# Kernel tuning notes

Hardware: AMD Instinct MI355X
Metric: run time of the kernel (lower is better)

The kernel has to match this reference:

```python
import jax, jax.numpy as jnp
import numpy as np

B, S = 64, 512
NQ, RAW, D, H, K = 10000, 256, 256, 64, 4  # vocab, raw emb, model emb, gru state, num_stages
LN_EPS = 1e-5


def setup_inputs() -> dict:
    key = jax.random.key(0)
    ks = jax.random.split(key, 30)
    def n(i, shape, s=0.02):
        return (jax.random.normal(ks[i], shape) * s).astype(jnp.float32)
    return {
        "q": jax.random.randint(ks[0], (B, S), 0, NQ, dtype=jnp.int32),
        "r": jax.random.randint(ks[1], (B, S), 0, 2, dtype=jnp.int32),
        # flattened 4-stage embedding table [NQ*4, RAW]
        "emb_table": n(2, (NQ * K, RAW)),
        # per-stage expert MLPs (weights stored as [in, out])
        "expert_w1": n(3, (K, RAW, RAW)), "expert_b1": n(4, (K, RAW)),
        "expert_w2": n(5, (K, RAW, D)),  "expert_b2": n(6, (K, D)),
        # router input adapter Linear(RAW*4 -> D)
        "adapter_w": n(7, (RAW * K, D)), "adapter_b": n(8, (D,)),
        # interaction reducer Linear(2D -> H)
        "reducer_w": n(9, (2 * D, H)), "reducer_b": n(10, (H,)),
        "start_token": jnp.zeros((1, 1, H), jnp.float32),
        # torch GRU params: [3H, in], gate order (r, z, n)
        "gru_w_ih": n(11, (3 * H, H)), "gru_w_hh": n(12, (3 * H, H)),
        "gru_b_ih": n(13, (3 * H,)),   "gru_b_hh": n(14, (3 * H,)),
        # gate Linear(D+H -> 4)
        "wgate_w": n(15, (D + H, K)), "wgate_b": n(16, (K,)),
        "ln_gamma": jnp.ones((D,), jnp.float32), "ln_beta": jnp.zeros((D,), jnp.float32),
        "resp_table": n(17, (2, D)),
        "proj_cor_w": n(18, (D, D)), "proj_cor_b": n(19, (D,)),
        "proj_inc_w": n(20, (D, D)), "proj_inc_b": n(21, (D,)),
    }


def _forward(q, r, emb_table, expert_w1, expert_b1, expert_w2, expert_b2,
             adapter_w, adapter_b, reducer_w, reducer_b, start_token,
             gru_w_ih, gru_w_hh, gru_b_ih, gru_b_hh, wgate_w, wgate_b,
             ln_gamma, ln_beta, resp_table, proj_cor_w, proj_cor_b,
             proj_inc_w, proj_inc_b):
    b, s = q.shape
    # 4-stage embedding lookup: indices q*4 + [0..3]
    stage_idx = q[..., None] * K + jnp.arange(K)          # [B,S,4]
    q_raw = emb_table[stage_idx]                          # [B,S,4,RAW]
    # smart summary (router input adapter), eval mode -> no dropout
    q_flat = q_raw.reshape(b, s, K * RAW)
    q_summary = jax.nn.relu(q_flat @ adapter_w + adapter_b)  # [B,S,D]
    r_emb = resp_table[r]                                    # [B,S,D]
    gru_in = jnp.concatenate([q_summary, r_emb], -1) @ reducer_w + reducer_b  # [B,S,H]
    start = jnp.broadcast_to(start_token, (b, 1, H))
    x = jnp.concatenate([start, gru_in[:, :-1]], axis=1)     # shifted [B,S,H]
    # GRU over time (torch gate order r,z,n)
    xg = x @ gru_w_ih.T + gru_b_ih                           # [B,S,3H]
    def step(h, xg_t):
        hg = h @ gru_w_hh.T + gru_b_hh
        xr, xz, xn = jnp.split(xg_t, 3, axis=-1)
        hr, hz, hn = jnp.split(hg, 3, axis=-1)
        rg = jax.nn.sigmoid(xr + hr)
        zg = jax.nn.sigmoid(xz + hz)
        ng = jnp.tanh(xn + rg * hn)
        h_new = (1.0 - zg) * ng + zg * h
        return h_new, h_new
    _, m = jax.lax.scan(step, jnp.zeros((b, H), x.dtype), xg.transpose(1, 0, 2))
    m_seq = m.transpose(1, 0, 2)                             # [B,S,H]
    # parallel experts (vectorized over the 4 stages)
    h1 = jax.nn.relu(jnp.einsum('bske,keh->bskh', q_raw, expert_w1) + expert_b1)
    experts = jnp.einsum('bskh,khd->bskd', h1, expert_w2) + expert_b2  # [B,S,4,D]
    # noisy routing (eval: no noise), top-1 mask, softmax gating
    logits = jnp.concatenate([q_summary, m_seq], -1) @ wgate_w + wgate_b  # [B,S,4]
    gate_probs = jax.nn.softmax(logits, axis=-1)
    top1 = jnp.argmax(logits, axis=-1)
    onehot = jax.nn.one_hot(top1, K, dtype=logits.dtype)
    masked = jnp.where(onehot > 0, logits, -jnp.inf)
    gate_w = jax.nn.softmax(masked, axis=-1)                 # one-hot for top_k=1
    combined = jnp.einsum('bskd,bsk->bsd', experts, gate_w)  # [B,S,D]
    # layer norm
    mu = combined.mean(-1, keepdims=True)
    var = combined.var(-1, keepdims=True)
    q_fused = ln_gamma * (combined - mu) * jax.lax.rsqrt(var + LN_EPS) + ln_beta
    emb_cor = q_fused @ proj_cor_w + proj_cor_b
    emb_inc = q_fused @ proj_inc_w + proj_inc_b
    rm = r[..., None].astype(q_fused.dtype)
    qa_fused = emb_cor * rm + emb_inc * (1.0 - rm)
    return q_fused, qa_fused, gate_probs


def reference(q, r, emb_table, expert_w1, expert_b1, expert_w2, expert_b2,
              adapter_w, adapter_b, reducer_w, reducer_b, start_token,
              gru_w_ih, gru_w_hh, gru_b_ih, gru_b_hh, wgate_w, wgate_b,
              ln_gamma, ln_beta, resp_table, proj_cor_w, proj_cor_b,
              proj_inc_w, proj_inc_b):
    q_fused, qa_fused, _ = _forward(q, r, emb_table, expert_w1, expert_b1,
                                    expert_w2, expert_b2, adapter_w, adapter_b,
                                    reducer_w, reducer_b, start_token,
                                    gru_w_ih, gru_w_hh, gru_b_ih, gru_b_hh,
                                    wgate_w, wgate_b, ln_gamma, ln_beta,
                                    resp_table, proj_cor_w, proj_cor_b,
                                    proj_inc_w, proj_inc_b)
    return (q_fused, qa_fused)
```

## Files before the change

### kernel.cpp

```cpp
#include <hip/hip_runtime.h>
#include <cstddef>


#define NQ 10000
#define TT 32768

typedef __attribute__((ext_vector_type(8))) short bf16x8;
typedef __attribute__((ext_vector_type(4))) float f32x4;

__device__ double g_qs  [NQ * 256];
__device__ double g_xgr [2 * 192];
__device__ float  g_xg0f[192];
__device__ float  g_xq2 [NQ * 384];
__device__ double g_lq  [NQ * 4];
__device__ float  g_m   [TT * 64];
__device__ int    g_top1[TT];
__device__ unsigned short g_w1t  [4 * 256 * 256];
__device__ unsigned short g_w2t  [4 * 256 * 256];
__device__ unsigned short g_projt[512 * 256];
__device__ unsigned short g_qf   [NQ * 4 * 256];

__device__ __forceinline__ float bf2f(unsigned short x) {
  return __uint_as_float(((unsigned)x) << 16);
}
__device__ __forceinline__ unsigned short f2bf(float f) {
  unsigned u = __float_as_uint(f);
  u += 0x7FFFu + ((u >> 16) & 1u);
  return (unsigned short)(u >> 16);
}
__device__ __forceinline__ f32x4 mfma16(bf16x8 a, bf16x8 b, f32x4 c) {
  return __builtin_amdgcn_mfma_f32_16x16x32_bf16(a, b, c, 0, 0, 0);
}
__device__ __forceinline__ void pkfma(float2& c, float2 a, float2 b) {
  asm("v_pk_fma_f32 %0, %1, %2, %0" : "+v"(c) : "v"(a), "v"(b));
}

__device__ __forceinline__ double fexp(double x) {
  const double L2E  = 1.4426950408889634074;
  const double LN2H = 6.93147180369123816490e-01;
  const double LN2L = 1.90821492927058770002e-10;
  double n = rint(x * L2E);
  int ni = (int)n;
  double r = fma(-n, LN2H, x);
  r = fma(-n, LN2L, r);
  double p = 2.7557319223985888e-07;
  p = fma(p, r, 2.7557319223985893e-06);
  p = fma(p, r, 2.4801587301587302e-05);
  p = fma(p, r, 1.9841269841269841e-04);
  p = fma(p, r, 1.3888888888888889e-03);
  p = fma(p, r, 8.3333333333333332e-03);
  p = fma(p, r, 4.1666666666666664e-02);
  p = fma(p, r, 1.6666666666666666e-01);
  p = fma(p, r, 0.5);
  p = fma(p, r, 1.0);
  p = fma(p, r, 1.0);
  return ldexp(p, ni);
}

__device__ __forceinline__ double tpoly(double p) {
  const double p2 = p * p;
  double t = -1382.0 / 155925.0;
  t = fma(t, p2, 62.0 / 2835.0);
  t = fma(t, p2, -17.0 / 315.0);
  t = fma(t, p2, 2.0 / 15.0);
  t = fma(t, p2, -1.0 / 3.0);
  t = fma(t, p2, 1.0);
  return p * t;
}

__global__ void __launch_bounds__(256) prep_kernel(
    const float* __restrict__ expert_w1, const float* __restrict__ expert_w2,
    const float* __restrict__ proj_cor_w, const float* __restrict__ proj_inc_w,
    const float* __restrict__ resp_table, const float* __restrict__ reducer_w,
    const float* __restrict__ reducer_b,  const float* __restrict__ start_token,
    const float* __restrict__ gru_w_ih,   const float* __restrict__ gru_b_ih)
{
  __shared__ double red2f[128];
  const int tid = threadIdx.x;
  if (blockIdx.x == 0) {
    if (tid < 128) {
      const int rr = tid >> 6, j = tid & 63;
      double acc = (double)reducer_b[j];
      for (int k = 0; k < 256; ++k)
        acc += (double)resp_table[rr * 256 + k] *
               (double)reducer_w[(256 + k) * 64 + j];
      red2f[tid] = acc;
    }
    __syncthreads();
    if (tid < 192) {
      const double bih = (double)gru_b_ih[tid];
      double a0 = bih, a1 = bih, a2 = bih;
      for (int j = 0; j < 64; ++j) {
        const double w = (double)gru_w_ih[tid * 64 + j];
        a0 += red2f[j] * w;
        a1 += red2f[64 + j] * w;
        a2 += (double)start_token[j] * w;
      }
      g_xgr[tid] = a0; g_xgr[192 + tid] = a1; g_xg0f[tid] = (float)a2;
    }
  }
  const int idx0 = blockIdx.x * 256 + tid;
  const int stride = gridDim.x * 256;
  for (int i = idx0; i < 4 * 256 * 256; i += stride) {
    const int e = i >> 16, rem = i & 65535, n = rem >> 8, k = rem & 255;
    g_w1t[i] = f2bf(expert_w1[e * 65536 + k * 256 + n]);
    g_w2t[i] = f2bf(expert_w2[e * 65536 + k * 256 + n]);
  }
  for (int i = idx0; i < 512 * 256; i += stride) {
    const int n = i >> 8, k = i & 255;
    g_projt[i] = f2bf((n < 256) ? proj_cor_w[k * 256 + n]
                                : proj_inc_w[k * 256 + (n - 256)]);
  }
}

__global__ void __launch_bounds__(256) qsk_kernel(
    const float* __restrict__ emb, const float* __restrict__ adapter_w,
    const float* __restrict__ adapter_b)
{
  __shared__ __align__(16) float As[64][33];
  __shared__ __align__(16) float Bs[32][65];
  const int tid = threadIdx.x;
  const int q0 = blockIdx.x * 64;
  const int n0 = blockIdx.y * 64;
  const int ty = tid >> 4, tx = tid & 15;

  double acc[4][4];
#pragma unroll
  for (int i = 0; i < 4; ++i)
#pragma unroll
    for (int j = 0; j < 4; ++j) acc[i][j] = 0.0;

  const int arow = tid >> 2, aks = (tid & 3) * 8;
  const int qa = min(q0 + arow, NQ - 1);
  const int bkk = tid >> 3, bns = (tid & 7) * 8;

  for (int kc = 0; kc < 1024; kc += 32) {
    f32x4 av0 = *(const f32x4*)(emb + (size_t)qa * 1024 + kc + aks);
    f32x4 av1 = *(const f32x4*)(emb + (size_t)qa * 1024 + kc + aks + 4);
    f32x4 bv0 = *(const f32x4*)(adapter_w + (size_t)(kc + bkk) * 256 + n0 + bns);
    f32x4 bv1 = *(const f32x4*)(adapter_w + (size_t)(kc + bkk) * 256 + n0 + bns + 4);
    __syncthreads();
#pragma unroll
    for (int i = 0; i < 4; ++i) { As[arow][aks + i] = av0[i]; As[arow][aks + 4 + i] = av1[i]; }
#pragma unroll
    for (int i = 0; i < 4; ++i) { Bs[bkk][bns + i] = bv0[i]; Bs[bkk][bns + 4 + i] = bv1[i]; }
    __syncthreads();
#pragma unroll 4
    for (int kk = 0; kk < 32; ++kk) {
      double a[4], b[4];
#pragma unroll
      for (int i = 0; i < 4; ++i) a[i] = (double)As[ty * 4 + i][kk];
#pragma unroll
      for (int j = 0; j < 4; ++j) b[j] = (double)Bs[kk][tx * 4 + j];
#pragma unroll
      for (int i = 0; i < 4; ++i)
#pragma unroll
        for (int j = 0; j < 4; ++j) acc[i][j] = fma(a[i], b[j], acc[i][j]);
    }
  }
#pragma unroll
  for (int i = 0; i < 4; ++i) {
    const int qrow = q0 + ty * 4 + i;
    if (qrow < NQ) {
#pragma unroll
      for (int j = 0; j < 4; ++j) {
        const int n = n0 + tx * 4 + j;
        double v = acc[i][j] + (double)adapter_b[n];
        g_qs[(size_t)qrow * 256 + n] = v > 0.0 ? v : 0.0;
      }
    }
  }
}

__global__ void __launch_bounds__(256) smallk_kernel(
    const float* __restrict__ reducer_w, const float* __restrict__ gru_w_ih,
    const float* __restrict__ wgate_w)
{
  __shared__ double qsr[256];
  __shared__ double ps[4][64];
  __shared__ double gi[64];
  const int tid = threadIdx.x;
  const int qq = blockIdx.x;
  qsr[tid] = g_qs[(size_t)qq * 256 + tid];
  __syncthreads();
  {
    const int j = tid & 63, h = tid >> 6;
    const int k0 = h * 64;
    double a0 = 0.0, a1 = 0.0, a2 = 0.0, a3 = 0.0;
    for (int k = 0; k < 64; k += 4) {
      a0 = fma(qsr[k0 + k + 0], (double)reducer_w[(k0 + k + 0) * 64 + j], a0);
      a1 = fma(qsr[k0 + k + 1], (double)reducer_w[(k0 + k + 1) * 64 + j], a1);
      a2 = fma(qsr[k0 + k + 2], (double)reducer_w[(k0 + k + 2) * 64 + j], a2);
      a3 = fma(qsr[k0 + k + 3], (double)reducer_w[(k0 + k + 3) * 64 + j], a3);
    }
    ps[h][j] = (a0 + a1) + (a2 + a3);
  }
  __syncthreads();
  if (tid < 64) gi[tid] = (ps[0][tid] + ps[1][tid]) + (ps[2][tid] + ps[3][tid]);
  if (tid >= 64 && tid < 68) {
    const int e = tid - 64;
    double a0 = 0.0, a1 = 0.0, a2 = 0.0, a3 = 0.0;
    for (int k = 0; k < 256; k += 4) {
      a0 = fma(qsr[k + 0], (double)wgate_w[(k + 0) * 4 + e], a0);
      a1 = fma(qsr[k + 1], (double)wgate_w[(k + 1) * 4 + e], a1);
      a2 = fma(qsr[k + 2], (double)wgate_w[(k + 2) * 4 + e], a2);
      a3 = fma(qsr[k + 3], (double)wgate_w[(k + 3) * 4 + e], a3);
    }
    g_lq[(size_t)qq * 4 + e] = (a0 + a1) + (a2 + a3);
  }
  __syncthreads();
  if (tid < 192) {
    double a0 = 0.0, a1 = 0.0, a2 = 0.0, a3 = 0.0;
    for (int k = 0; k < 64; k += 4) {
      a0 = fma(gi[k + 0], (double)gru_w_ih[tid * 64 + k + 0], a0);
      a1 = fma(gi[k + 1], (double)gru_w_ih[tid * 64 + k + 1], a1);
      a2 = fma(gi[k + 2], (double)gru_w_ih[tid * 64 + k + 2], a2);
      a3 = fma(gi[k + 3], (double)gru_w_ih[tid * 64 + k + 3], a3);
    }
    const double s = (a0 + a1) + (a2 + a3);
    g_xq2[(size_t)qq * 384 + tid]       = (float)(s + g_xgr[tid]);
    g_xq2[(size_t)qq * 384 + 192 + tid] = (float)(s + g_xgr[192 + tid]);
  }
}

__global__ void __attribute__((amdgpu_waves_per_eu(1, 1)))
__launch_bounds__(128, 1) gru_kernel(
    const int* __restrict__ q, const int* __restrict__ r,
    const float* __restrict__ whh, const float* __restrict__ bhh)
{
  __shared__ __align__(16) float HF[2][68];
  const int tid = threadIdx.x;
  const int b = blockIdx.x;
  const int wv = tid >> 6;
  const int l = tid & 63;
  const int p = l >> 1;
  const int half = l & 1;
  const int j = wv * 32 + p;
  const int k0 = half * 32;

  float2 Wr[16], Wz[16], Wn[16];
#pragma unroll
  for (int i = 0; i < 16; ++i) {
    Wr[i] = *(const float2*)(whh + (size_t)(0 * 64 + j) * 64 + k0 + 2 * i);
    Wz[i] = *(const float2*)(whh + (size_t)(1 * 64 + j) * 64 + k0 + 2 * i);
    Wn[i] = *(const float2*)(whh + (size_t)(2 * 64 + j) * 64 + k0 + 2 * i);
  }
#pragma unroll
  for (int i = 0; i < 16; ++i) {
    asm volatile("" : "+v"(Wr[i]));
    asm volatile("" : "+v"(Wz[i]));
    asm volatile("" : "+v"(Wn[i]));
  }
  const double br = (double)bhh[j];
  const double bz = (double)bhh[64 + j];
  const double bn = (double)bhh[128 + j];

  float cx0 = g_xg0f[j], cx1 = g_xg0f[64 + j], cx2 = g_xg0f[128 + j];
  int qA = q[b * 512], rA = r[b * 512];

  const int jpad = j + ((j >> 5) << 2);
  if (tid < 64) {
    const int tp = tid + ((tid >> 5) << 2);
    HF[0][tp] = 0.f;
  }
  double hd = 0.0;
  asm volatile("s_waitcnt lgkmcnt(0)\n\ts_barrier" ::: "memory");

  for (int t = 0; t < 512; ++t) {
    float nx0 = 0.f, nx1 = 0.f, nx2 = 0.f;
    int qB = qA, rB = rA;
    if (t < 511) {
      const size_t base = (size_t)(qA * 2 + rA) * 192 + j;
      nx0 = g_xq2[base];
      nx1 = g_xq2[base + 64];
      nx2 = g_xq2[base + 128];
      const int tk = min(t + 1, 510);
      qB = q[b * 512 + tk];
      rB = r[b * 512 + tk];
    }

    float2 ar = {0.f, 0.f}, az = {0.f, 0.f}, an = {0.f, 0.f};
    {
      const float4* hp = (const float4*)&HF[t & 1][half * 36];
#pragma unroll
      for (int g = 0; g < 8; ++g) {
        const float4 t4 = hp[g];
        const float2 hA = make_float2(t4.x, t4.y);
        const float2 hB = make_float2(t4.z, t4.w);
        pkfma(ar, Wr[2 * g], hA); pkfma(ar, Wr[2 * g + 1], hB);
        pkfma(az, Wz[2 * g], hA); pkfma(az, Wz[2 * g + 1], hB);
        pkfma(an, Wn[2 * g], hA); pkfma(an, Wn[2 * g + 1], hB);
      }
    }
    const float srh = ar.x + ar.y;
    const float szh = az.x + az.y;
    const float snh = an.x + an.y;
    const float sro = __shfl_xor(srh, 1);
    const float szo = __shfl_xor(szh, 1);
    const float sno = __shfl_xor(snh, 1);
    const double hr = br + ((double)srh + (double)sro);
    const double hz = bz + ((double)szh + (double)szo);
    const double hn = bn + ((double)snh + (double)sno);
    const double pr = (double)cx0 + hr, pz = (double)cx1 + hz;
    const double xn = (double)cx2;
    double rg = fma(0.5, tpoly(0.5 * pr), 0.5);
    double zg = fma(0.5, tpoly(0.5 * pz), 0.5);
    double pre = fma(rg, hn, xn);
    double ng = tpoly(pre);
    const bool bad = (fabs(pr) > 0.5) | (fabs(pz) > 0.5) | (fabs(pre) > 0.25);
    if (bad) {
      rg = 1.0 / (1.0 + fexp(-pr));
      zg = 1.0 / (1.0 + fexp(-pz));
      pre = fma(rg, hn, xn);
      ng = 1.0 - 2.0 / (fexp(pre + pre) + 1.0);
    }
    const double hnew = fma(zg, hd - ng, ng);
    hd = hnew;
    const float hnf = (float)hnew;
    if (half == 0) {
      HF[(t & 1) ^ 1][jpad] = hnf;
      g_m[((size_t)b * 512 + t) * 64 + j] = hnf;
    }
    asm volatile("s_waitcnt lgkmcnt(0)\n\ts_barrier" ::: "memory");

    cx0 = nx0; cx1 = nx1; cx2 = nx2;
    qA = qB; rA = rB;
  }
}

__global__ void __launch_bounds__(256) top1_kernel(
    const int* __restrict__ q,
    const float* __restrict__ wgate_w, const float* __restrict__ wgate_b)
{
  __shared__ double w2[256];
  const int tid = threadIdx.x;
  w2[tid] = (double)wgate_w[1024 + tid];
  __syncthreads();
  const int t = blockIdx.x * 256 + tid;
  const int qv = q[t];
  double l0 = g_lq[(size_t)qv * 4 + 0] + (double)wgate_b[0];
  double l1 = g_lq[(size_t)qv * 4 + 1] + (double)wgate_b[1];
  double l2 = g_lq[(size_t)qv * 4 + 2] + (double)wgate_b[2];
  double l3 = g_lq[(size_t)qv * 4 + 3] + (double)wgate_b[3];
  const f32x4* mr4 = (const f32x4*)(g_m + (size_t)t * 64);
#pragma unroll 4
  for (int jj = 0; jj < 16; ++jj) {
    const f32x4 mv4 = mr4[jj];
#pragma unroll
    for (int c = 0; c < 4; ++c) {
      const double mv = (double)mv4[c];
      const int k = (jj * 4 + c) * 4;
      l0 = fma(mv, w2[k + 0], l0);
      l1 = fma(mv, w2[k + 1], l1);
      l2 = fma(mv, w2[k + 2], l2);
      l3 = fma(mv, w2[k + 3], l3);
    }
  }
  int bi = 0; double bvv = l0;
  if (l1 > bvv) { bvv = l1; bi = 1; }
  if (l2 > bvv) { bvv = l2; bi = 2; }
  if (l3 > bvv) { bvv = l3; bi = 3; }
  g_top1[t] = bi;
}

__global__ void __launch_bounds__(128) kernelE(
    const float* __restrict__ emb,
    const float* __restrict__ b1, const float* __restrict__ b2,
    const float* __restrict__ lng, const float* __restrict__ lnb)
{
  __shared__ __align__(16) unsigned short QR[32 * 264];
  __shared__ __align__(16) unsigned short H1[32 * 264];
  __shared__ __align__(16) unsigned short EO[32 * 264];
  const int tid = threadIdx.x;
  const int t0 = blockIdx.x * 32;
  const int e  = blockIdx.y;
  const int w = tid >> 6;
  const int lane = tid & 63;
  const int l15 = lane & 15;
  const int quad = lane >> 4;

  for (int c = 0; c < 16; ++c) {
    const int idx = c * 128 + tid;
    const int row = idx >> 6, col4 = idx & 63;
    const int qv = min(t0 + row, NQ - 1);
    f32x4 v = *(const f32x4*)(emb + (size_t)qv * 1024 + e * 256 + col4 * 4);
    unsigned a = ((unsigned)f2bf(v[1]) << 16) | f2bf(v[0]);
    unsigned bb = ((unsigned)f2bf(v[3]) << 16) | f2bf(v[2]);
    *(uint2*)&QR[row * 264 + col4 * 4] = make_uint2(a, bb);
  }
  __syncthreads();

  const f32x4 z4 = {0.f, 0.f, 0.f, 0.f};
  const int n0 = w * 128;

  f32x4 acc[2][8];
#pragma unroll
  for (int a = 0; a < 2; ++a)
#pragma unroll
    for (int bq = 0; bq < 8; ++bq) acc[a][bq] = z4;
#pragma unroll
  for (int ks = 0; ks < 8; ++ks) {
    const int koff = ks * 32 + quad * 8;
    bf16x8 a0 = *(const bf16x8*)&QR[l15 * 264 + koff];
    bf16x8 a1 = *(const bf16x8*)&QR[(16 + l15) * 264 + koff];
#pragma unroll
    for (int nt = 0; nt < 8; ++nt) {
      bf16x8 bbv = *(const bf16x8*)(g_w1t + (size_t)e * 65536 +
                                    (size_t)(n0 + nt * 16 + l15) * 256 + koff);
      acc[0][nt] = mfma16(a0, bbv, acc[0][nt]);
      acc[1][nt] = mfma16(a1, bbv, acc[1][nt]);
    }
  }
#pragma unroll
  for (int nt = 0; nt < 8; ++nt) {
    const int n = n0 + nt * 16 + l15;
    const float b1v = b1[e * 256 + n];
#pragma unroll
    for (int mt = 0; mt < 2; ++mt)
#pragma unroll
      for (int rg = 0; rg < 4; ++rg) {
        const int m = mt * 16 + quad * 4 + rg;
        H1[m * 264 + n] = f2bf(fmaxf(acc[mt][nt][rg] + b1v, 0.f));
      }
  }
  __syncthreads();

  f32x4 acc2[2][8];
#pragma unroll
  for (int a = 0; a < 2; ++a)
#pragma unroll
    for (int bq = 0; bq < 8; ++bq) acc2[a][bq] = z4;
#pragma unroll
  for (int ks = 0; ks < 8; ++ks) {
    const int koff = ks * 32 + quad * 8;
    bf16x8 a0 = *(const bf16x8*)&H1[l15 * 264 + koff];
    bf16x8 a1 = *(const bf16x8*)&H1[(16 + l15) * 264 + koff];
#pragma unroll
    for (int nt = 0; nt < 8; ++nt) {
      bf16x8 bbv = *(const bf16x8*)(g_w2t + (size_t)e * 65536 +
                                    (size_t)(n0 + nt * 16 + l15) * 256 + koff);
      acc2[0][nt] = mfma16(a0, bbv, acc2[0][nt]);
      acc2[1][nt] = mfma16(a1, bbv, acc2[1][nt]);
    }
  }
#pragma unroll
  for (int nt = 0; nt < 8; ++nt) {
    const int n = n0 + nt * 16 + l15;
    const float b2v = b2[e * 256 + n];
#pragma unroll
    for (int mt = 0; mt < 2; ++mt)
#pragma unroll
      for (int rg = 0; rg < 4; ++rg) {
        const int m = mt * 16 + quad * 4 + rg;
        EO[m * 264 + n] = f2bf(acc2[mt][nt][rg] + b2v);
      }
  }
  __syncthreads();

  {
    const int m = tid >> 2;
    const int sub = tid & 3;
    float sx = 0.f, sxx = 0.f;
#pragma unroll
    for (int i = 0; i < 8; ++i) {
      bf16x8 v = *(const bf16x8*)&EO[m * 264 + sub * 64 + i * 8];
#pragma unroll
      for (int c = 0; c < 8; ++c) {
        const float f = bf2f((unsigned short)v[c]);
        sx += f; sxx += f * f;
      }
    }
    sx += __shfl_xor(sx, 1); sxx += __shfl_xor(sxx, 1);
    sx += __shfl_xor(sx, 2); sxx += __shfl_xor(sxx, 2);
    const float mu = sx * (1.f / 256.f);
    const float var = sxx * (1.f / 256.f) - mu * mu;
    const float inv = 1.f / sqrtf(var + 1e-5f);
    if (t0 + m < NQ) {
      const size_t base = ((size_t)(t0 + m) * 4 + e) * 256;
#pragma unroll
      for (int i = 0; i < 8; ++i) {
        const int dbase = sub * 64 + i * 8;
        bf16x8 v = *(const bf16x8*)&EO[m * 264 + dbase];
        bf16x8 ov;
#pragma unroll
        for (int c = 0; c < 8; ++c) {
          const int d = dbase + c;
          const float f = bf2f((unsigned short)v[c]);
          ov[c] = (short)f2bf(lng[d] * (f - mu) * inv + lnb[d]);
        }
        *(bf16x8*)(g_qf + base + dbase) = ov;
      }
    }
  }
}

__global__ void __launch_bounds__(128) kernelF(
    const int* __restrict__ q, const int* __restrict__ r,
    const float* __restrict__ pcb, const float* __restrict__ pib,
    float* __restrict__ out)
{
  __shared__ __align__(16) unsigned short QF[32 * 264];
  __shared__ int rv_l[32];
  const int tid = threadIdx.x;
  const int t0 = blockIdx.x * 32;
  const int w = tid >> 6;
  const int lane = tid & 63;
  const int l15 = lane & 15;
  const int quad = lane >> 4;
  if (tid < 32) rv_l[tid] = r[t0 + tid];
  __syncthreads();

  {
    const int m = tid >> 2;
    const size_t row = ((size_t)q[t0 + m] * 4 + g_top1[t0 + m]) * 256;
#pragma unroll
    for (int i = 0; i < 8; ++i) {
      const int dbase = (tid & 3) * 64 + i * 8;
      bf16x8 v = *(const bf16x8*)(g_qf + row + dbase);
      *(bf16x8*)&QF[m * 264 + dbase] = v;
      f32x4 f0, f1;
#pragma unroll
      for (int c = 0; c < 4; ++c) f0[c] = bf2f((unsigned short)v[c]);
#pragma unroll
      for (int c = 0; c < 4; ++c) f1[c] = bf2f((unsigned short)v[4 + c]);
      *(f32x4*)(out + (size_t)(t0 + m) * 256 + dbase) = f0;
      *(f32x4*)(out + (size_t)(t0 + m) * 256 + dbase + 4) = f1;
    }
  }
  __syncthreads();

  const f32x4 z4 = {0.f, 0.f, 0.f, 0.f};
  const int n0 = w * 128;
  for (int ph = 0; ph < 2; ++ph) {
    f32x4 acc[2][8];
#pragma unroll
    for (int a = 0; a < 2; ++a)
#pragma unroll
      for (int bq = 0; bq < 8; ++bq) acc[a][bq] = z4;
#pragma unroll
    for (int ks = 0; ks < 8; ++ks) {
      const int koff = ks * 32 + quad * 8;
      bf16x8 a0 = *(const bf16x8*)&QF[l15 * 264 + koff];
      bf16x8 a1 = *(const bf16x8*)&QF[(16 + l15) * 264 + koff];
#pragma unroll
      for (int nt = 0; nt < 8; ++nt) {
        bf16x8 bbv = *(const bf16x8*)(g_projt +
            (size_t)(ph * 256 + n0 + nt * 16 + l15) * 256 + koff);
        acc[0][nt] = mfma16(a0, bbv, acc[0][nt]);
        acc[1][nt] = mfma16(a1, bbv, acc[1][nt]);
      }
    }
    const float* pbb = ph ? pib : pcb;
    const int want = ph ? 0 : 1;
#pragma unroll
    for (int nt = 0; nt < 8; ++nt) {
      const int n = n0 + nt * 16 + l15;
      const float pbv = pbb[n];
#pragma unroll
      for (int mt = 0; mt < 2; ++mt)
#pragma unroll
        for (int rg = 0; rg < 4; ++rg) {
          const int m = mt * 16 + quad * 4 + rg;
          if (rv_l[m] == want)
            out[(size_t)TT * 256 + (size_t)(t0 + m) * 256 + n] =
                acc[mt][nt][rg] + pbv;
        }
    }
  }
}

extern "C" void kernel_launch(void* const* d_in, const int* in_sizes, int n_in,
                              void* d_out, int out_size, void* d_ws, size_t ws_size,
                              hipStream_t stream)
{
  const int*   q   = (const int*)d_in[0];
  const int*   r   = (const int*)d_in[1];
  const float* emb = (const float*)d_in[2];
  const float* ew1 = (const float*)d_in[3];
  const float* eb1 = (const float*)d_in[4];
  const float* ew2 = (const float*)d_in[5];
  const float* eb2 = (const float*)d_in[6];
  const float* aw  = (const float*)d_in[7];
  const float* ab  = (const float*)d_in[8];
  const float* rw  = (const float*)d_in[9];
  const float* rb  = (const float*)d_in[10];
  const float* st  = (const float*)d_in[11];
  const float* wih = (const float*)d_in[12];
  const float* whh = (const float*)d_in[13];
  const float* bih = (const float*)d_in[14];
  const float* bhh = (const float*)d_in[15];
  const float* wgw = (const float*)d_in[16];
  const float* wgb = (const float*)d_in[17];
  const float* lng = (const float*)d_in[18];
  const float* lnb = (const float*)d_in[19];
  const float* resp= (const float*)d_in[20];
  const float* pcw = (const float*)d_in[21];
  const float* pcb = (const float*)d_in[22];
  const float* piw = (const float*)d_in[23];
  const float* pib = (const float*)d_in[24];
  float* out = (float*)d_out;
  (void)bih; (void)in_sizes; (void)n_in; (void)d_ws; (void)ws_size; (void)out_size;

  prep_kernel<<<64, 256, 0, stream>>>(ew1, ew2, pcw, piw, resp, rw, rb, st, wih, bih);
  qsk_kernel<<<dim3(157, 4), 256, 0, stream>>>(emb, aw, ab);
  smallk_kernel<<<NQ, 256, 0, stream>>>(rw, wih, wgw);
  gru_kernel<<<64, 128, 0, stream>>>(q, r, whh, bhh);
  top1_kernel<<<128, 256, 0, stream>>>(q, wgw, wgb);
  kernelE<<<dim3(313, 4), 128, 0, stream>>>(emb, eb1, eb2, lng, lnb);
  kernelF<<<1024, 128, 0, stream>>>(q, r, pcb, pib, out);
}
```

Baseline: 856.1 us.

## Fuse expert MLP blocks into GRU kernel and merge prep with qsk

Merges the expert-MLP/LayerNorm kernel into the GRU kernel as extra blocks, so the latency-bound serial recurrence on 64 blocks overlaps with the parallel MLP work on otherwise idle CUs. Also merges the weight-prep and adapter GEMM kernels into one launch with block-index dispatch. In exchange, every block carries the union of shared memory and the GRU's one-wave-per-EU register bounds, which may reduce occupancy for the MLP blocks.

```diff
diff --git a/kernel.cpp b/kernel.cpp
--- a/kernel.cpp
+++ b/kernel.cpp
@@ -68,60 +68,61 @@
   return p * t;
 }
 
-__global__ void __launch_bounds__(256) prep_kernel(
+__global__ void __launch_bounds__(256) prepqsk_kernel(
     const float* __restrict__ expert_w1, const float* __restrict__ expert_w2,
     const float* __restrict__ proj_cor_w, const float* __restrict__ proj_inc_w,
     const float* __restrict__ resp_table, const float* __restrict__ reducer_w,
     const float* __restrict__ reducer_b,  const float* __restrict__ start_token,
-    const float* __restrict__ gru_w_ih,   const float* __restrict__ gru_b_ih)
-{
-  __shared__ double red2f[128];
-  const int tid = threadIdx.x;
-  if (blockIdx.x == 0) {
-    if (tid < 128) {
-      const int rr = tid >> 6, j = tid & 63;
-      double acc = (double)reducer_b[j];
-      for (int k = 0; k < 256; ++k)
-        acc += (double)resp_table[rr * 256 + k] *
-               (double)reducer_w[(256 + k) * 64 + j];
-      red2f[tid] = acc;
-    }
-    __syncthreads();
-    if (tid < 192) {
-      const double bih = (double)gru_b_ih[tid];
-      double a0 = bih, a1 = bih, a2 = bih;
-      for (int j = 0; j < 64; ++j) {
-        const double w = (double)gru_w_ih[tid * 64 + j];
-        a0 += red2f[j] * w;
-        a1 += red2f[64 + j] * w;
-        a2 += (double)start_token[j] * w;
-      }
-      g_xgr[tid] = a0; g_xgr[192 + tid] = a1; g_xg0f[tid] = (float)a2;
-    }
-  }
-  const int idx0 = blockIdx.x * 256 + tid;
-  const int stride = gridDim.x * 256;
-  for (int i = idx0; i < 4 * 256 * 256; i += stride) {
-    const int e = i >> 16, rem = i & 65535, n = rem >> 8, k = rem & 255;
-    g_w1t[i] = f2bf(expert_w1[e * 65536 + k * 256 + n]);
-    g_w2t[i] = f2bf(expert_w2[e * 65536 + k * 256 + n]);
-  }
-  for (int i = idx0; i < 512 * 256; i += stride) {
-    const int n = i >> 8, k = i & 255;
-    g_projt[i] = f2bf((n < 256) ? proj_cor_w[k * 256 + n]
-                                : proj_inc_w[k * 256 + (n - 256)]);
-  }
-}
-
-__global__ void __launch_bounds__(256) qsk_kernel(
+    const float* __restrict__ gru_w_ih,   const float* __restrict__ gru_b_ih,
     const float* __restrict__ emb, const float* __restrict__ adapter_w,
     const float* __restrict__ adapter_b)
 {
+  __shared__ double red2f[128];
   __shared__ __align__(16) float As[64][33];
   __shared__ __align__(16) float Bs[32][65];
   const int tid = threadIdx.x;
-  const int q0 = blockIdx.x * 64;
-  const int n0 = blockIdx.y * 64;
+
+  if (blockIdx.x < 64) {
+    if (blockIdx.x == 0) {
+      if (tid < 128) {
+        const int rr = tid >> 6, j = tid & 63;
+        double acc = (double)reducer_b[j];
+        for (int k = 0; k < 256; ++k)
+          acc += (double)resp_table[rr * 256 + k] *
+                 (double)reducer_w[(256 + k) * 64 + j];
+        red2f[tid] = acc;
+      }
+      __syncthreads();
+      if (tid < 192) {
+        const double bih = (double)gru_b_ih[tid];
+        double a0 = bih, a1 = bih, a2 = bih;
+        for (int j = 0; j < 64; ++j) {
+          const double w = (double)gru_w_ih[tid * 64 + j];
+          a0 += red2f[j] * w;
+          a1 += red2f[64 + j] * w;
+          a2 += (double)start_token[j] * w;
+        }
+        g_xgr[tid] = a0; g_xgr[192 + tid] = a1; g_xg0f[tid] = (float)a2;
+      }
+    }
+    const int idx0 = blockIdx.x * 256 + tid;
+    const int stride = 64 * 256;
+    for (int i = idx0; i < 4 * 256 * 256; i += stride) {
+      const int e = i >> 16, rem = i & 65535, n = rem >> 8, k = rem & 255;
+      g_w1t[i] = f2bf(expert_w1[e * 65536 + k * 256 + n]);
+      g_w2t[i] = f2bf(expert_w2[e * 65536 + k * 256 + n]);
+    }
+    for (int i = idx0; i < 512 * 256; i += stride) {
+      const int n = i >> 8, k = i & 255;
+      g_projt[i] = f2bf((n < 256) ? proj_cor_w[k * 256 + n]
+                                  : proj_inc_w[k * 256 + (n - 256)]);
+    }
+    return;
+  }
+
+  const int bq = blockIdx.x - 64;
+  const int q0 = (bq >> 2) * 64;
+  const int n0 = (bq & 3) * 64;
   const int ty = tid >> 4, tx = tid & 15;
 
   double acc[4][4];
@@ -224,107 +225,239 @@
 }
 
 __global__ void __attribute__((amdgpu_waves_per_eu(1, 1)))
-__launch_bounds__(128, 1) gru_kernel(
+__launch_bounds__(128, 1) gruE_kernel(
     const int* __restrict__ q, const int* __restrict__ r,
-    const float* __restrict__ whh, const float* __restrict__ bhh)
+    const float* __restrict__ whh, const float* __restrict__ bhh,
+    const float* __restrict__ emb,
+    const float* __restrict__ b1, const float* __restrict__ b2,
+    const float* __restrict__ lng, const float* __restrict__ lnb)
 {
   __shared__ __align__(16) float HF[2][68];
+  __shared__ __align__(16) unsigned short QR[32 * 264];
+  __shared__ __align__(16) unsigned short H1[32 * 264];
+  __shared__ __align__(16) unsigned short EO[32 * 264];
   const int tid = threadIdx.x;
-  const int b = blockIdx.x;
-  const int wv = tid >> 6;
-  const int l = tid & 63;
-  const int p = l >> 1;
-  const int half = l & 1;
-  const int j = wv * 32 + p;
-  const int k0 = half * 32;
-
-  float2 Wr[16], Wz[16], Wn[16];
-#pragma unroll
-  for (int i = 0; i < 16; ++i) {
-    Wr[i] = *(const float2*)(whh + (size_t)(0 * 64 + j) * 64 + k0 + 2 * i);
-    Wz[i] = *(const float2*)(whh + (size_t)(1 * 64 + j) * 64 + k0 + 2 * i);
-    Wn[i] = *(const float2*)(whh + (size_t)(2 * 64 + j) * 64 + k0 + 2 * i);
-  }
-#pragma unroll
-  for (int i = 0; i < 16; ++i) {
-    asm volatile("" : "+v"(Wr[i]));
-    asm volatile("" : "+v"(Wz[i]));
-    asm volatile("" : "+v"(Wn[i]));
-  }
-  const double br = (double)bhh[j];
-  const double bz = (double)bhh[64 + j];
-  const double bn = (double)bhh[128 + j];
-
-  float cx0 = g_xg0f[j], cx1 = g_xg0f[64 + j], cx2 = g_xg0f[128 + j];
-  int qA = q[b * 512], rA = r[b * 512];
-
-  const int jpad = j + ((j >> 5) << 2);
-  if (tid < 64) {
-    const int tp = tid + ((tid >> 5) << 2);
-    HF[0][tp] = 0.f;
-  }
-  double hd = 0.0;
-  asm volatile("s_waitcnt lgkmcnt(0)\n\ts_barrier" ::: "memory");
-
-  for (int t = 0; t < 512; ++t) {
-    float nx0 = 0.f, nx1 = 0.f, nx2 = 0.f;
-    int qB = qA, rB = rA;
-    if (t < 511) {
-      const size_t base = (size_t)(qA * 2 + rA) * 192 + j;
-      nx0 = g_xq2[base];
-      nx1 = g_xq2[base + 64];
-      nx2 = g_xq2[base + 128];
-      const int tk = min(t + 1, 510);
-      qB = q[b * 512 + tk];
-      rB = r[b * 512 + tk];
-    }
-
-    float2 ar = {0.f, 0.f}, az = {0.f, 0.f}, an = {0.f, 0.f};
-    {
-      const float4* hp = (const float4*)&HF[t & 1][half * 36];
-#pragma unroll
-      for (int g = 0; g < 8; ++g) {
-        const float4 t4 = hp[g];
-        const float2 hA = make_float2(t4.x, t4.y);
-        const float2 hB = make_float2(t4.z, t4.w);
-        pkfma(ar, Wr[2 * g], hA); pkfma(ar, Wr[2 * g + 1], hB);
-        pkfma(az, Wz[2 * g], hA); pkfma(az, Wz[2 * g + 1], hB);
-        pkfma(an, Wn[2 * g], hA); pkfma(an, Wn[2 * g + 1], hB);
-      }
-    }
-    const float srh = ar.x + ar.y;
-    const float szh = az.x + az.y;
-    const float snh = an.x + an.y;
-    const float sro = __shfl_xor(srh, 1);
-    const float szo = __shfl_xor(szh, 1);
-    const float sno = __shfl_xor(snh, 1);
-    const double hr = br + ((double)srh + (double)sro);
-    const double hz = bz + ((double)szh + (double)szo);
-    const double hn = bn + ((double)snh + (double)sno);
-    const double pr = (double)cx0 + hr, pz = (double)cx1 + hz;
-    const double xn = (double)cx2;
-    double rg = fma(0.5, tpoly(0.5 * pr), 0.5);
-    double zg = fma(0.5, tpoly(0.5 * pz), 0.5);
-    double pre = fma(rg, hn, xn);
-    double ng = tpoly(pre);
-    const bool bad = (fabs(pr) > 0.5) | (fabs(pz) > 0.5) | (fabs(pre) > 0.25);
-    if (bad) {
-      rg = 1.0 / (1.0 + fexp(-pr));
-      zg = 1.0 / (1.0 + fexp(-pz));
-      pre = fma(rg, hn, xn);
-      ng = 1.0 - 2.0 / (fexp(pre + pre) + 1.0);
-    }
-    const double hnew = fma(zg, hd - ng, ng);
-    hd = hnew;
-    const float hnf = (float)hnew;
-    if (half == 0) {
-      HF[(t & 1) ^ 1][jpad] = hnf;
-      g_m[((size_t)b * 512 + t) * 64 + j] = hnf;
-    }
+
+  if (blockIdx.x < 64) {
+    const int b = blockIdx.x;
+    const int wv = tid >> 6;
+    const int l = tid & 63;
+    const int p = l >> 1;
+    const int half = l & 1;
+    const int j = wv * 32 + p;
+    const int k0 = half * 32;
+
+    float2 Wr[16], Wz[16], Wn[16];
+#pragma unroll
+    for (int i = 0; i < 16; ++i) {
+      Wr[i] = *(const float2*)(whh + (size_t)(0 * 64 + j) * 64 + k0 + 2 * i);
+      Wz[i] = *(const float2*)(whh + (size_t)(1 * 64 + j) * 64 + k0 + 2 * i);
+      Wn[i] = *(const float2*)(whh + (size_t)(2 * 64 + j) * 64 + k0 + 2 * i);
+    }
+#pragma unroll
+    for (int i = 0; i < 16; ++i) {
+      asm volatile("" : "+v"(Wr[i]));
+      asm volatile("" : "+v"(Wz[i]));
+      asm volatile("" : "+v"(Wn[i]));
+    }
+    const double br = (double)bhh[j];
+    const double bz = (double)bhh[64 + j];
+    const double bn = (double)bhh[128 + j];
+
+    float cx0 = g_xg0f[j], cx1 = g_xg0f[64 + j], cx2 = g_xg0f[128 + j];
+    int qA = q[b * 512], rA = r[b * 512];
+
+    const int jpad = j + ((j >> 5) << 2);
+    if (tid < 64) {
+      const int tp = tid + ((tid >> 5) << 2);
+      HF[0][tp] = 0.f;
+    }
+    double hd = 0.0;
     asm volatile("s_waitcnt lgkmcnt(0)\n\ts_barrier" ::: "memory");
 
-    cx0 = nx0; cx1 = nx1; cx2 = nx2;
-    qA = qB; rA = rB;
+    for (int t = 0; t < 512; ++t) {
+      float nx0 = 0.f, nx1 = 0.f, nx2 = 0.f;
+      int qB = qA, rB = rA;
+      if (t < 511) {
+        const size_t base = (size_t)(qA * 2 + rA) * 192 + j;
+        nx0 = g_xq2[base];
+        nx1 = g_xq2[base + 64];
+        nx2 = g_xq2[base + 128];
+        const int tk = min(t + 1, 510);
+        qB = q[b * 512 + tk];
+        rB = r[b * 512 + tk];
+      }
+
+      float2 ar = {0.f, 0.f}, az = {0.f, 0.f}, an = {0.f, 0.f};
+      {
+        const float4* hp = (const float4*)&HF[t & 1][half * 36];
+#pragma unroll
+        for (int g = 0; g < 8; ++g) {
+          const float4 t4 = hp[g];
+          const float2 hA = make_float2(t4.x, t4.y);
+          const float2 hB = make_float2(t4.z, t4.w);
+          pkfma(ar, Wr[2 * g], hA); pkfma(ar, Wr[2 * g + 1], hB);
+          pkfma(az, Wz[2 * g], hA); pkfma(az, Wz[2 * g + 1], hB);
+          pkfma(an, Wn[2 * g], hA); pkfma(an, Wn[2 * g + 1], hB);
+        }
+      }
+      const float srh = ar.x + ar.y;
+      const float szh = az.x + az.y;
+      const float snh = an.x + an.y;
+      const float sro = __shfl_xor(srh, 1);
+      const float szo = __shfl_xor(szh, 1);
+      const float sno = __shfl_xor(snh, 1);
+      const double hr = br + ((double)srh + (double)sro);
+      const double hz = bz + ((double)szh + (double)szo);
+      const double hn = bn + ((double)snh + (double)sno);
+      const double pr = (double)cx0 + hr, pz = (double)cx1 + hz;
+      const double xn = (double)cx2;
+      double rg = fma(0.5, tpoly(0.5 * pr), 0.5);
+      double zg = fma(0.5, tpoly(0.5 * pz), 0.5);
+      double pre = fma(rg, hn, xn);
+      double ng = tpoly(pre);
+      const bool bad = (fabs(pr) > 0.5) | (fabs(pz) > 0.5) | (fabs(pre) > 0.25);
+      if (bad) {
+        rg = 1.0 / (1.0 + fexp(-pr));
+        zg = 1.0 / (1.0 + fexp(-pz));
+        pre = fma(rg, hn, xn);
+        ng = 1.0 - 2.0 / (fexp(pre + pre) + 1.0);
+      }
+      const double hnew = fma(zg, hd - ng, ng);
+      hd = hnew;
+      const float hnf = (float)hnew;
+      if (half == 0) {
+        HF[(t & 1) ^ 1][jpad] = hnf;
+        g_m[((size_t)b * 512 + t) * 64 + j] = hnf;
+      }
+      asm volatile("s_waitcnt lgkmcnt(0)\n\ts_barrier" ::: "memory");
+
+      cx0 = nx0; cx1 = nx1; cx2 = nx2;
+      qA = qB; rA = rB;
+    }
+    return;
+  }
+
+  const int bx = blockIdx.x - 64;
+  const int e  = bx & 3;
+  const int t0 = (bx >> 2) * 32;
+  const int w = tid >> 6;
+  const int lane = tid & 63;
+  const int l15 = lane & 15;
+  const int quad = lane >> 4;
+
+  for (int c = 0; c < 16; ++c) {
+    const int idx = c * 128 + tid;
+    const int row = idx >> 6, col4 = idx & 63;
+    const int qv = min(t0 + row, NQ - 1);
+    f32x4 v = *(const f32x4*)(emb + (size_t)qv * 1024 + e * 256 + col4 * 4);
+    unsigned a = ((unsigned)f2bf(v[1]) << 16) | f2bf(v[0]);
+    unsigned bb = ((unsigned)f2bf(v[3]) << 16) | f2bf(v[2]);
+    *(uint2*)&QR[row * 264 + col4 * 4] = make_uint2(a, bb);
+  }
+  __syncthreads();
+
+  const f32x4 z4 = {0.f, 0.f, 0.f, 0.f};
+  const int n0 = w * 128;
+
+  f32x4 acc[2][8];
+#pragma unroll
+  for (int a = 0; a < 2; ++a)
+#pragma unroll
+    for (int bq = 0; bq < 8; ++bq) acc[a][bq] = z4;
+#pragma unroll
+  for (int ks = 0; ks < 8; ++ks) {
+    const int koff = ks * 32 + quad * 8;
+    bf16x8 a0 = *(const bf16x8*)&QR[l15 * 264 + koff];
+    bf16x8 a1 = *(const bf16x8*)&QR[(16 + l15) * 264 + koff];
+#pragma unroll
+    for (int nt = 0; nt < 8; ++nt) {
+      bf16x8 bbv = *(const bf16x8*)(g_w1t + (size_t)e * 65536 +
+                                    (size_t)(n0 + nt * 16 + l15) * 256 + koff);
+      acc[0][nt] = mfma16(a0, bbv, acc[0][nt]);
+      acc[1][nt] = mfma16(a1, bbv, acc[1][nt]);
+    }
+  }
+#pragma unroll
+  for (int nt = 0; nt < 8; ++nt) {
+    const int n = n0 + nt * 16 + l15;
+    const float b1v = b1[e * 256 + n];
+#pragma unroll
+    for (int mt = 0; mt < 2; ++mt)
+#pragma unroll
+      for (int rg = 0; rg < 4; ++rg) {
+        const int m = mt * 16 + quad * 4 + rg;
+        H1[m * 264 + n] = f2bf(fmaxf(acc[mt][nt][rg] + b1v, 0.f));
+      }
+  }
+  __syncthreads();
+
+  f32x4 acc2[2][8];
+#pragma unroll
+  for (int a = 0; a < 2; ++a)
+#pragma unroll
+    for (int bq = 0; bq < 8; ++bq) acc2[a][bq] = z4;
+#pragma unroll
+  for (int ks = 0; ks < 8; ++ks) {
+    const int koff = ks * 32 + quad * 8;
+    bf16x8 a0 = *(const bf16x8*)&H1[l15 * 264 + koff];
+    bf16x8 a1 = *(const bf16x8*)&H1[(16 + l15) * 264 + koff];
+#pragma unroll
+    for (int nt = 0; nt < 8; ++nt) {
+      bf16x8 bbv = *(const bf16x8*)(g_w2t + (size_t)e * 65536 +
+                                    (size_t)(n0 + nt * 16 + l15) * 256 + koff);
+      acc2[0][nt] = mfma16(a0, bbv, acc2[0][nt]);
+      acc2[1][nt] = mfma16(a1, bbv, acc2[1][nt]);
+    }
+  }
+#pragma unroll
+  for (int nt = 0; nt < 8; ++nt) {
+    const int n = n0 + nt * 16 + l15;
+    const float b2v = b2[e * 256 + n];
+#pragma unroll
+    for (int mt = 0; mt < 2; ++mt)
+#pragma unroll
+      for (int rg = 0; rg < 4; ++rg) {
+        const int m = mt * 16 + quad * 4 + rg;
+        EO[m * 264 + n] = f2bf(acc2[mt][nt][rg] + b2v);
+      }
+  }
+  __syncthreads();
+
+  {
+    const int m = tid >> 2;
+    const int sub = tid & 3;
+    float sx = 0.f, sxx = 0.f;
+#pragma unroll
+    for (int i = 0; i < 8; ++i) {
+      bf16x8 v = *(const bf16x8*)&EO[m * 264 + sub * 64 + i * 8];
+#pragma unroll
+      for (int c = 0; c < 8; ++c) {
+        const float f = bf2f((unsigned short)v[c]);
+        sx += f; sxx += f * f;
+      }
+    }
+    sx += __shfl_xor(sx, 1); sxx += __shfl_xor(sxx, 1);
+    sx += __shfl_xor(sx, 2); sxx += __shfl_xor(sxx, 2);
+    const float mu = sx * (1.f / 256.f);
+    const float var = sxx * (1.f / 256.f) - mu * mu;
+    const float inv = 1.f / sqrtf(var + 1e-5f);
+    if (t0 + m < NQ) {
+      const size_t base = ((size_t)(t0 + m) * 4 + e) * 256;
+#pragma unroll
+      for (int i = 0; i < 8; ++i) {
+        const int dbase = sub * 64 + i * 8;
+        bf16x8 v = *(const bf16x8*)&EO[m * 264 + dbase];
+        bf16x8 ov;
+#pragma unroll
+        for (int c = 0; c < 8; ++c) {
+          const int d = dbase + c;
+          const float f = bf2f((unsigned short)v[c]);
+          ov[c] = (short)f2bf(lng[d] * (f - mu) * inv + lnb[d]);
+        }
+        *(bf16x8*)(g_qf + base + dbase) = ov;
+      }
+    }
   }
 }
 
@@ -361,137 +494,6 @@
   if (l2 > bvv) { bvv = l2; bi = 2; }
   if (l3 > bvv) { bvv = l3; bi = 3; }
   g_top1[t] = bi;
-}
-
-__global__ void __launch_bounds__(128) kernelE(
-    const float* __restrict__ emb,
-    const float* __restrict__ b1, const float* __restrict__ b2,
-    const float* __restrict__ lng, const float* __restrict__ lnb)
-{
-  __shared__ __align__(16) unsigned short QR[32 * 264];
-  __shared__ __align__(16) unsigned short H1[32 * 264];
-  __shared__ __align__(16) unsigned short EO[32 * 264];
-  const int tid = threadIdx.x;
-  const int t0 = blockIdx.x * 32;
-  const int e  = blockIdx.y;
-  const int w = tid >> 6;
-  const int lane = tid & 63;
-  const int l15 = lane & 15;
-  const int quad = lane >> 4;
-
-  for (int c = 0; c < 16; ++c) {
-    const int idx = c * 128 + tid;
-    const int row = idx >> 6, col4 = idx & 63;
-    const int qv = min(t0 + row, NQ - 1);
-    f32x4 v = *(const f32x4*)(emb + (size_t)qv * 1024 + e * 256 + col4 * 4);
-    unsigned a = ((unsigned)f2bf(v[1]) << 16) | f2bf(v[0]);
-    unsigned bb = ((unsigned)f2bf(v[3]) << 16) | f2bf(v[2]);
-    *(uint2*)&QR[row * 264 + col4 * 4] = make_uint2(a, bb);
-  }
-  __syncthreads();
-
-  const f32x4 z4 = {0.f, 0.f, 0.f, 0.f};
-  const int n0 = w * 128;
-
-  f32x4 acc[2][8];
-#pragma unroll
-  for (int a = 0; a < 2; ++a)
-#pragma unroll
-    for (int bq = 0; bq < 8; ++bq) acc[a][bq] = z4;
-#pragma unroll
-  for (int ks = 0; ks < 8; ++ks) {
-    const int koff = ks * 32 + quad * 8;
-    bf16x8 a0 = *(const bf16x8*)&QR[l15 * 264 + koff];
-    bf16x8 a1 = *(const bf16x8*)&QR[(16 + l15) * 264 + koff];
-#pragma unroll
-    for (int nt = 0; nt < 8; ++nt) {
-      bf16x8 bbv = *(const bf16x8*)(g_w1t + (size_t)e * 65536 +
-                                    (size_t)(n0 + nt * 16 + l15) * 256 + koff);
-      acc[0][nt] = mfma16(a0, bbv, acc[0][nt]);
-      acc[1][nt] = mfma16(a1, bbv, acc[1][nt]);
-    }
-  }
-#pragma unroll
-  for (int nt = 0; nt < 8; ++nt) {
-    const int n = n0 + nt * 16 + l15;
-    const float b1v = b1[e * 256 + n];
-#pragma unroll
-    for (int mt = 0; mt < 2; ++mt)
-#pragma unroll
-      for (int rg = 0; rg < 4; ++rg) {
-        const int m = mt * 16 + quad * 4 + rg;
-        H1[m * 264 + n] = f2bf(fmaxf(acc[mt][nt][rg] + b1v, 0.f));
-      }
-  }
-  __syncthreads();
-
-  f32x4 acc2[2][8];
-#pragma unroll
-  for (int a = 0; a < 2; ++a)
-#pragma unroll
-    for (int bq = 0; bq < 8; ++bq) acc2[a][bq] = z4;
-#pragma unroll
-  for (int ks = 0; ks < 8; ++ks) {
-    const int koff = ks * 32 + quad * 8;
-    bf16x8 a0 = *(const bf16x8*)&H1[l15 * 264 + koff];
-    bf16x8 a1 = *(const bf16x8*)&H1[(16 + l15) * 264 + koff];
-#pragma unroll
-    for (int nt = 0; nt < 8; ++nt) {
-      bf16x8 bbv = *(const bf16x8*)(g_w2t + (size_t)e * 65536 +
-                                    (size_t)(n0 + nt * 16 + l15) * 256 + koff);
-      acc2[0][nt] = mfma16(a0, bbv, acc2[0][nt]);
-      acc2[1][nt] = mfma16(a1, bbv, acc2[1][nt]);
-    }
-  }
-#pragma unroll
-  for (int nt = 0; nt < 8; ++nt) {
-    const int n = n0 + nt * 16 + l15;
-    const float b2v = b2[e * 256 + n];
-#pragma unroll
-    for (int mt = 0; mt < 2; ++mt)
-#pragma unroll
-      for (int rg = 0; rg < 4; ++rg) {
-        const int m = mt * 16 + quad * 4 + rg;
-        EO[m * 264 + n] = f2bf(acc2[mt][nt][rg] + b2v);
-      }
-  }
-  __syncthreads();
-
-  {
-    const int m = tid >> 2;
-    const int sub = tid & 3;
-    float sx = 0.f, sxx = 0.f;
-#pragma unroll
-    for (int i = 0; i < 8; ++i) {
-      bf16x8 v = *(const bf16x8*)&EO[m * 264 + sub * 64 + i * 8];
-#pragma unroll
-      for (int c = 0; c < 8; ++c) {
-        const float f = bf2f((unsigned short)v[c]);
-        sx += f; sxx += f * f;
-      }
-    }
-    sx += __shfl_xor(sx, 1); sxx += __shfl_xor(sxx, 1);
-    sx += __shfl_xor(sx, 2); sxx += __shfl_xor(sxx, 2);
-    const float mu = sx * (1.f / 256.f);
-    const float var = sxx * (1.f / 256.f) - mu * mu;
-    const float inv = 1.f / sqrtf(var + 1e-5f);
-    if (t0 + m < NQ) {
-      const size_t base = ((size_t)(t0 + m) * 4 + e) * 256;
-#pragma unroll
-      for (int i = 0; i < 8; ++i) {
-        const int dbase = sub * 64 + i * 8;
-        bf16x8 v = *(const bf16x8*)&EO[m * 264 + dbase];
-        bf16x8 ov;
-#pragma unroll
-        for (int c = 0; c < 8; ++c) {
-          const int d = dbase + c;
-          const float f = bf2f((unsigned short)v[c]);
-          ov[c] = (short)f2bf(lng[d] * (f - mu) * inv + lnb[d]);
-        }
-        *(bf16x8*)(g_qf + base + dbase) = ov;
-      }
-    }
-  }
 }
 
 __global__ void __launch_bounds__(128) kernelF(
@@ -601,11 +603,11 @@
   float* out = (float*)d_out;
   (void)bih; (void)in_sizes; (void)n_in; (void)d_ws; (void)ws_size; (void)out_size;
 
-  prep_kernel<<<64, 256, 0, stream>>>(ew1, ew2, pcw, piw, resp, rw, rb, st, wih, bih);
-  qsk_kernel<<<dim3(157, 4), 256, 0, stream>>>(emb, aw, ab);
+  prepqsk_kernel<<<692, 256, 0, stream>>>(ew1, ew2, pcw, piw, resp, rw, rb, st,
+                                          wih, bih, emb, aw, ab);
   smallk_kernel<<<NQ, 256, 0, stream>>>(rw, wih, wgw);
-  gru_kernel<<<64, 128, 0, stream>>>(q, r, whh, bhh);
+  gruE_kernel<<<64 + 313 * 4, 128, 0, stream>>>(q, r, whh, bhh,
+                                                emb, eb1, eb2, lng, lnb);
   top1_kernel<<<128, 256, 0, stream>>>(q, wgw, wgb);
-  kernelE<<<dim3(313, 4), 128, 0, stream>>>(emb, eb1, eb2, lng, lnb);
   kernelF<<<1024, 128, 0, stream>>>(q, r, pcb, pib, out);
 }
```

Measured after the change: 778.8 us. 1.1x faster.
